# Kernel tuning notes

Hardware: AMD Instinct MI355X
Metric: run time of the kernel (lower is better)

## Reference

```python
import jax, jax.numpy as jnp
import numpy as np

EPS = 1e-6
HEAD_DIM = 64
N_Q = 16
N_KV = 2

def setup_inputs() -> dict:
    key = jax.random.key(0)
    ks = jax.random.split(key, 4)
    H = 1024
    x = jax.random.normal(ks[0], (4, 8192, H), dtype=jnp.float32)
    ln_weight = jnp.zeros((H,), dtype=jnp.float32)  # Gemma param; scale is (1 + w)
    wq = jax.random.normal(ks[1], (H, HEAD_DIM * N_Q), dtype=jnp.float32) / np.sqrt(H)
    wk = jax.random.normal(ks[2], (H, HEAD_DIM * N_KV), dtype=jnp.float32) / np.sqrt(H)
    wv = jax.random.normal(ks[3], (H, HEAD_DIM * N_KV), dtype=jnp.float32) / np.sqrt(H)
    return {"x": x, "ln_weight": ln_weight, "wq": wq, "wk": wk, "wv": wv}

def gemma_rms_norm(x, w):
    xf = x.astype(jnp.float32)
    h = xf * jax.lax.rsqrt(jnp.mean(xf * xf, axis=-1, keepdims=True) + EPS)
    return (h * (1.0 + w.astype(jnp.float32))).astype(x.dtype)

def reference(x, ln_weight, wq, wk, wv):
    # Gemma RMSNorm prologue, then three linear projections (no bias).
    h = gemma_rms_norm(x, ln_weight)            # [B, S, H]
    q = jnp.einsum('bsh,hd->bsd', h, wq)        # [B, S, nq*d]
    k = jnp.einsum('bsh,hd->bsd', h, wk)        # [B, S, nkv*d]
    v = jnp.einsum('bsh,hd->bsd', h, wv)
    B, S = x.shape[0], x.shape[1]
    q = q.reshape(B, S, N_Q, HEAD_DIM)
    k = k.reshape(B, S, N_KV, HEAD_DIM)
    v = v.reshape(B, S, N_KV, HEAD_DIM)
    return (q, k, v)
```

## Files before the change

kernel.cpp:

```cpp
#include <hip/hip_runtime.h>
#include <hip/hip_bf16.h>

typedef __attribute__((ext_vector_type(4))) float f32x4;
typedef __attribute__((ext_vector_type(8))) short bf16x8;

#define H 1024
#define NTOT 1280
#define BM 128
#define BN 256
#define BK 64
#define NKT 16
#define NTILES 5

static __device__ __forceinline__ unsigned short f2bf(float f) {
    __hip_bfloat16 b = __float2bfloat16(f);
    return __builtin_bit_cast(unsigned short, b);
}

#define GLOAD_LDS16(g, l)                                                     \
    __builtin_amdgcn_global_load_lds(                                         \
        (const __attribute__((address_space(1))) void*)(g),                   \
        (__attribute__((address_space(3))) void*)(l), 16, 0, 0)

__global__ __launch_bounds__(256) void k_rms(const float* __restrict__ x,
                                             __hip_bfloat16* __restrict__ h) {
    const int wave = threadIdx.x >> 6;
    const int lane = threadIdx.x & 63;
    const size_t row = (size_t)blockIdx.x * 4 + wave;

    const float4* xr = (const float4*)(x + row * H);
    float4 v[4];
    float ss = 0.f;
#pragma unroll
    for (int i = 0; i < 4; ++i) {
        v[i] = xr[lane + 64 * i];
        ss += v[i].x * v[i].x + v[i].y * v[i].y + v[i].z * v[i].z + v[i].w * v[i].w;
    }
#pragma unroll
    for (int o = 1; o < 64; o <<= 1) ss += __shfl_xor(ss, o);
    const float sc = rsqrtf(ss * (1.0f / H) + 1e-6f);

    ushort4* hr = (ushort4*)(h + row * H);
#pragma unroll
    for (int i = 0; i < 4; ++i) {
        ushort4 o4;
        o4.x = f2bf(v[i].x * sc);
        o4.y = f2bf(v[i].y * sc);
        o4.z = f2bf(v[i].z * sc);
        o4.w = f2bf(v[i].w * sc);
        hr[lane + 64 * i] = o4;
    }
}

__global__ __launch_bounds__(256) void k_wprep(const float* __restrict__ wq,
                                               const float* __restrict__ wk,
                                               const float* __restrict__ wv,
                                               const float* __restrict__ lnw,
                                               __hip_bfloat16* __restrict__ Bt) {
    __shared__ float l[64][65];
    const int t = threadIdx.x;
    const int kt = blockIdx.x & 15;
    const int ntl = blockIdx.x >> 4;
    const int k0 = kt * 64, n0 = ntl * 64;
    const float* src; int ldn, nb;
    if (n0 < 1024)      { src = wq; ldn = 1024; nb = n0; }
    else if (n0 < 1152) { src = wk; ldn = 128;  nb = n0 - 1024; }
    else                { src = wv; ldn = 128;  nb = n0 - 1152; }
    const int nl = t & 63, kl = t >> 6;
#pragma unroll
    for (int i = 0; i < 16; ++i) {
        const int k = kl + i * 4;
        l[k][nl] = (1.0f + lnw[k0 + k]) * src[(size_t)(k0 + k) * ldn + nb + nl];
    }
    __syncthreads();
    const int k2 = t & 63, n2 = t >> 6;
#pragma unroll
    for (int i = 0; i < 16; ++i) {
        const int n = n2 + i * 4;
        Bt[(size_t)(n0 + n) * 1024 + k0 + k2] = __float2bfloat16(l[k2][n]);
    }
}

__global__ __launch_bounds__(512, 2) void k_gemm(const __hip_bfloat16* __restrict__ A,
                                                 const __hip_bfloat16* __restrict__ Bt,
                                                 float* __restrict__ out, int rows) {
    __shared__ __align__(16) char smem[98304];

    const int tid = threadIdx.x;
    const int lane = tid & 63;
    const int wid = tid >> 6;
    const int wm = wid >> 1;
    const int wn = wid & 1;

    const int cpx = gridDim.x >> 3;
    const int wg = (blockIdx.x & 7) * cpx + (blockIdx.x >> 3);
    const int nt = wg % NTILES;
    const int mt = wg / NTILES;
    const size_t m0 = (size_t)mt * BM;

    const int cswz = ((tid & 7) * 16) ^ (((tid >> 3) & 7) << 4);
    const char* aG = (const char*)A + (m0 + (tid >> 3)) * (size_t)(H * 2) + cswz;
    const char* bG = (const char*)Bt + ((size_t)nt * BN + (tid >> 3)) * (size_t)(H * 2) + cswz;

#define STAGE_A2(buf, kt)                                                     \
    { GLOAD_LDS16(aG + (size_t)(kt) * 128,                                    \
                  smem + (buf) * 49152 + tid * 16);                           \
      GLOAD_LDS16(aG + (size_t)(kt) * 128 + (size_t)64 * (H * 2),             \
                  smem + (buf) * 49152 + 8192 + tid * 16); }
#define STAGE_B02(buf, kt)                                                    \
    { GLOAD_LDS16(bG + (size_t)(kt) * 128,                                    \
                  smem + (buf) * 49152 + 16384 + tid * 16);                   \
      GLOAD_LDS16(bG + (size_t)(kt) * 128 + (size_t)128 * (H * 2),            \
                  smem + (buf) * 49152 + 16384 + 16384 + tid * 16); }
#define STAGE_B13(buf, kt)                                                    \
    { GLOAD_LDS16(bG + (size_t)(kt) * 128 + (size_t)64 * (H * 2),             \
                  smem + (buf) * 49152 + 16384 + 8192 + tid * 16);            \
      GLOAD_LDS16(bG + (size_t)(kt) * 128 + (size_t)192 * (H * 2),            \
                  smem + (buf) * 49152 + 16384 + 24576 + tid * 16); }

    const int rowA = wm * 32 + (lane & 15);
    const int rowB = wn * 128 + (lane & 15);
    const int xm = (lane & 7) << 4;
    const int c0 = (((lane >> 4) * 16)) ^ xm;
    const int c1 = (64 + ((lane >> 4) * 16)) ^ xm;

    f32x4 acc[2][8] = {};

#define MFMAP(AK0, AK1, B0, B1, NIOFF)                                        \
    _Pragma("unroll") for (int mi = 0; mi < 2; ++mi)                          \
        _Pragma("unroll") for (int ni = 0; ni < 4; ++ni)                      \
            acc[mi][(NIOFF) + ni] = __builtin_amdgcn_mfma_f32_16x16x32_bf16(  \
                AK0[mi], B0[ni], acc[mi][(NIOFF) + ni], 0, 0, 0);             \
    _Pragma("unroll") for (int mi = 0; mi < 2; ++mi)                          \
        _Pragma("unroll") for (int ni = 0; ni < 4; ++ni)                      \
            acc[mi][(NIOFF) + ni] = __builtin_amdgcn_mfma_f32_16x16x32_bf16(  \
                AK1[mi], B1[ni], acc[mi][(NIOFF) + ni], 0, 0, 0);

#define TILE(cur, kt, CARRY, DS, VM)                                          \
    {                                                                         \
        const char* aL = smem + (cur) * 49152;                                \
        const char* bL = aL + 16384;                                          \
                                                            \
        if (CARRY) STAGE_B13((cur) ^ 1, (kt) + 1);                            \
        bf16x8 ak0[2], ak1[2], b0k0[4], b0k1[4];                              \
        _Pragma("unroll") for (int mi = 0; mi < 2; ++mi) {                    \
            ak0[mi] = *(const bf16x8*)(aL + (rowA + mi * 16) * 128 + c0);     \
            ak1[mi] = *(const bf16x8*)(aL + (rowA + mi * 16) * 128 + c1);     \
        }                                                                     \
        _Pragma("unroll") for (int ni = 0; ni < 4; ++ni) {                    \
            b0k0[ni] = *(const bf16x8*)(bL + (rowB + ni * 16) * 128 + c0);    \
            b0k1[ni] = *(const bf16x8*)(bL + (rowB + ni * 16) * 128 + c1);    \
        }                                                                     \
        asm volatile("s_waitcnt lgkmcnt(8)" ::: "memory");                    \
        __builtin_amdgcn_s_barrier();                                         \
        asm volatile("s_waitcnt lgkmcnt(0)" ::: "memory");                    \
        __builtin_amdgcn_s_setprio(1);                                        \
        MFMAP(ak0, ak1, b0k0, b0k1, 0);                                       \
        __builtin_amdgcn_s_setprio(0);                                        \
        __builtin_amdgcn_s_barrier();                                         \
                                                            \
        if (DS) { STAGE_A2(cur, (kt) + 2); STAGE_B02(cur, (kt) + 2); }        \
        bf16x8 b1k0[4], b1k1[4];                                              \
        _Pragma("unroll") for (int ni = 0; ni < 4; ++ni) {                    \
            b1k0[ni] = *(const bf16x8*)(bL + (rowB + 64 + ni * 16) * 128 + c0); \
            b1k1[ni] = *(const bf16x8*)(bL + (rowB + 64 + ni * 16) * 128 + c1); \
        }                                                                     \
        __builtin_amdgcn_s_barrier();                                         \
        asm volatile("s_waitcnt lgkmcnt(0)" ::: "memory");                    \
        __builtin_amdgcn_s_setprio(1);                                        \
        MFMAP(ak0, ak1, b1k0, b1k1, 4);                                       \
        __builtin_amdgcn_s_setprio(0);                                        \
        asm volatile("s_waitcnt vmcnt(" VM ")" ::: "memory");                 \
        __builtin_amdgcn_sched_barrier(0);                                    \
        __builtin_amdgcn_s_barrier();                                         \
        __builtin_amdgcn_sched_barrier(0);                                    \
    }

    STAGE_A2(0, 0); STAGE_B02(0, 0); STAGE_B13(0, 0);
    STAGE_A2(1, 1); STAGE_B02(1, 1); STAGE_B13(1, 1);
    asm volatile("s_waitcnt vmcnt(6)" ::: "memory");
    __builtin_amdgcn_sched_barrier(0);
    __builtin_amdgcn_s_barrier();
    __builtin_amdgcn_sched_barrier(0);

    TILE(0, 0, 0, 1, "4");
    TILE(1, 1, 1, 1, "4");
    for (int kt = 2; kt <= 12; kt += 2) {
        TILE(0, kt, 1, 1, "4");
        TILE(1, kt + 1, 1, 1, "4");
    }
    TILE(0, 14, 1, 0, "0");
    TILE(1, 15, 0, 0, "0");

    const size_t QSZ = (size_t)rows * 1024;
    const size_t KSZ = (size_t)rows * 128;
    const int colg0 = nt * BN + wn * 128;
    float* op;
    int ldc, cb0;
    if (colg0 < 1024)      { op = out;             ldc = 1024; cb0 = colg0; }
    else if (colg0 < 1152) { op = out + QSZ;       ldc = 128;  cb0 = colg0 - 1024; }
    else                   { op = out + QSZ + KSZ; ldc = 128;  cb0 = colg0 - 1152; }

    const size_t r0 = m0 + wm * 32 + ((lane >> 4) * 4);
    const int cc0 = cb0 + (lane & 15);
#pragma unroll
    for (int mi = 0; mi < 2; ++mi)
#pragma unroll
        for (int ni = 0; ni < 8; ++ni)
#pragma unroll
            for (int r = 0; r < 4; ++r)
                op[(r0 + mi * 16 + r) * (size_t)ldc + cc0 + ni * 16] = acc[mi][ni][r];
}

extern "C" void kernel_launch(void* const* d_in, const int* in_sizes, int n_in,
                              void* d_out, int out_size, void* d_ws, size_t ws_size,
                              hipStream_t stream) {
    const float* x   = (const float*)d_in[0];
    const float* lnw = (const float*)d_in[1];
    const float* wq  = (const float*)d_in[2];
    const float* wk  = (const float*)d_in[3];
    const float* wv  = (const float*)d_in[4];
    float* out = (float*)d_out;

    const int rows = in_sizes[0] / H;

    __hip_bfloat16* Bt = (__hip_bfloat16*)d_ws;
    __hip_bfloat16* h  = (__hip_bfloat16*)((char*)d_ws + (size_t)NTOT * H * 2);

    k_wprep<<<320, 256, 0, stream>>>(wq, wk, wv, lnw, Bt);
    k_rms<<<rows / 4, 256, 0, stream>>>(x, h);
    k_gemm<<<(rows / BM) * NTILES, 512, 0, stream>>>(h, Bt, out, rows);
}
```

Baseline: 151.7 us.

## Use 256x256 tiles with A staged in LDS and B loaded directly into registers

```diff
diff --git a/kernel.cpp b/kernel.cpp
--- a/kernel.cpp
+++ b/kernel.cpp
@@ -6,7 +6,7 @@
 
 #define H 1024
 #define NTOT 1280
-#define BM 128
+#define BM 256
 #define BN 256
 #define BK 64
 #define NKT 16
@@ -84,13 +84,13 @@
 __global__ __launch_bounds__(512, 2) void k_gemm(const __hip_bfloat16* __restrict__ A,
                                                  const __hip_bfloat16* __restrict__ Bt,
                                                  float* __restrict__ out, int rows) {
-    __shared__ __align__(16) char smem[98304];
+    __shared__ __align__(16) char smem[65536];
 
     const int tid = threadIdx.x;
     const int lane = tid & 63;
     const int wid = tid >> 6;
-    const int wm = wid >> 1;
-    const int wn = wid & 1;
+    const int wm = wid >> 2;
+    const int wn = wid & 3;
 
     const int cpx = gridDim.x >> 3;
     const int wg = (blockIdx.x & 7) * cpx + (blockIdx.x >> 3);
@@ -100,113 +100,92 @@
 
     const int cswz = ((tid & 7) * 16) ^ (((tid >> 3) & 7) << 4);
     const char* aG = (const char*)A + (m0 + (tid >> 3)) * (size_t)(H * 2) + cswz;
-    const char* bG = (const char*)Bt + ((size_t)nt * BN + (tid >> 3)) * (size_t)(H * 2) + cswz;
-
-#define STAGE_A2(buf, kt)                                                     \
-    { GLOAD_LDS16(aG + (size_t)(kt) * 128,                                    \
-                  smem + (buf) * 49152 + tid * 16);                           \
-      GLOAD_LDS16(aG + (size_t)(kt) * 128 + (size_t)64 * (H * 2),             \
-                  smem + (buf) * 49152 + 8192 + tid * 16); }
-#define STAGE_B02(buf, kt)                                                    \
-    { GLOAD_LDS16(bG + (size_t)(kt) * 128,                                    \
-                  smem + (buf) * 49152 + 16384 + tid * 16);                   \
-      GLOAD_LDS16(bG + (size_t)(kt) * 128 + (size_t)128 * (H * 2),            \
-                  smem + (buf) * 49152 + 16384 + 16384 + tid * 16); }
-#define STAGE_B13(buf, kt)                                                    \
-    { GLOAD_LDS16(bG + (size_t)(kt) * 128 + (size_t)64 * (H * 2),             \
-                  smem + (buf) * 49152 + 16384 + 8192 + tid * 16);            \
-      GLOAD_LDS16(bG + (size_t)(kt) * 128 + (size_t)192 * (H * 2),            \
-                  smem + (buf) * 49152 + 16384 + 24576 + tid * 16); }
-
-    const int rowA = wm * 32 + (lane & 15);
-    const int rowB = wn * 128 + (lane & 15);
+
+#define STAGE_A(buf, kt)                                                      \
+    _Pragma("unroll") for (int q = 0; q < 4; ++q)                             \
+        GLOAD_LDS16(aG + (size_t)(kt) * 128 + (size_t)q * 64 * (H * 2),       \
+                    smem + (buf) * 32768 + q * 8192 + tid * 16);
+
+    const short* bGr = (const short*)Bt
+        + ((size_t)nt * BN + wn * 64 + (lane & 15)) * (size_t)H
+        + (lane >> 4) * 8;
+
+#define BLOAD(dst, kt)                                                        \
+    _Pragma("unroll") for (int ni = 0; ni < 4; ++ni)                          \
+        _Pragma("unroll") for (int kk = 0; kk < 2; ++kk)                      \
+            dst[ni * 2 + kk] = *(const bf16x8*)(bGr + ni * 16 * H + kk * 32   \
+                                                + (size_t)(kt) * 64);
+
+    const int rowA = wm * 128 + (lane & 15);
     const int xm = (lane & 7) << 4;
     const int c0 = (((lane >> 4) * 16)) ^ xm;
     const int c1 = (64 + ((lane >> 4) * 16)) ^ xm;
 
-    f32x4 acc[2][8] = {};
-
-#define MFMAP(AK0, AK1, B0, B1, NIOFF)                                        \
-    _Pragma("unroll") for (int mi = 0; mi < 2; ++mi)                          \
-        _Pragma("unroll") for (int ni = 0; ni < 4; ++ni)                      \
-            acc[mi][(NIOFF) + ni] = __builtin_amdgcn_mfma_f32_16x16x32_bf16(  \
-                AK0[mi], B0[ni], acc[mi][(NIOFF) + ni], 0, 0, 0);             \
-    _Pragma("unroll") for (int mi = 0; mi < 2; ++mi)                          \
-        _Pragma("unroll") for (int ni = 0; ni < 4; ++ni)                      \
-            acc[mi][(NIOFF) + ni] = __builtin_amdgcn_mfma_f32_16x16x32_bf16(  \
-                AK1[mi], B1[ni], acc[mi][(NIOFF) + ni], 0, 0, 0);
-
-#define TILE(cur, kt, CARRY, DS, VM)                                          \
+    f32x4 acc[8][4] = {};
+
+#define TILE(cur, kt, BN_, DS_, bcur, bnext)                                  \
     {                                                                         \
-        const char* aL = smem + (cur) * 49152;                                \
-        const char* bL = aL + 16384;                                          \
-                                                            \
-        if (CARRY) STAGE_B13((cur) ^ 1, (kt) + 1);                            \
-        bf16x8 ak0[2], ak1[2], b0k0[4], b0k1[4];                              \
-        _Pragma("unroll") for (int mi = 0; mi < 2; ++mi) {                    \
-            ak0[mi] = *(const bf16x8*)(aL + (rowA + mi * 16) * 128 + c0);     \
-            ak1[mi] = *(const bf16x8*)(aL + (rowA + mi * 16) * 128 + c1);     \
-        }                                                                     \
-        _Pragma("unroll") for (int ni = 0; ni < 4; ++ni) {                    \
-            b0k0[ni] = *(const bf16x8*)(bL + (rowB + ni * 16) * 128 + c0);    \
-            b0k1[ni] = *(const bf16x8*)(bL + (rowB + ni * 16) * 128 + c1);    \
-        }                                                                     \
-        asm volatile("s_waitcnt lgkmcnt(8)" ::: "memory");                    \
-        __builtin_amdgcn_s_barrier();                                         \
+        if (BN_) BLOAD(bnext, (kt) + 1);                                      \
+        const char* aL = smem + (cur) * 32768;                                \
+        bf16x8 af[8];                                                         \
+        _Pragma("unroll") for (int mi = 0; mi < 8; ++mi)                      \
+            af[mi] = *(const bf16x8*)(aL + (rowA + mi * 16) * 128 + c0);      \
         asm volatile("s_waitcnt lgkmcnt(0)" ::: "memory");                    \
         __builtin_amdgcn_s_setprio(1);                                        \
-        MFMAP(ak0, ak1, b0k0, b0k1, 0);                                       \
+        _Pragma("unroll") for (int mi = 0; mi < 8; ++mi)                      \
+            _Pragma("unroll") for (int ni = 0; ni < 4; ++ni)                  \
+                acc[mi][ni] = __builtin_amdgcn_mfma_f32_16x16x32_bf16(        \
+                    af[mi], bcur[ni * 2 + 0], acc[mi][ni], 0, 0, 0);          \
         __builtin_amdgcn_s_setprio(0);                                        \
-        __builtin_amdgcn_s_barrier();                                         \
-                                                            \
-        if (DS) { STAGE_A2(cur, (kt) + 2); STAGE_B02(cur, (kt) + 2); }        \
-        bf16x8 b1k0[4], b1k1[4];                                              \
-        _Pragma("unroll") for (int ni = 0; ni < 4; ++ni) {                    \
-            b1k0[ni] = *(const bf16x8*)(bL + (rowB + 64 + ni * 16) * 128 + c0); \
-            b1k1[ni] = *(const bf16x8*)(bL + (rowB + 64 + ni * 16) * 128 + c1); \
-        }                                                                     \
-        __builtin_amdgcn_s_barrier();                                         \
+        _Pragma("unroll") for (int mi = 0; mi < 8; ++mi)                      \
+            af[mi] = *(const bf16x8*)(aL + (rowA + mi * 16) * 128 + c1);      \
         asm volatile("s_waitcnt lgkmcnt(0)" ::: "memory");                    \
         __builtin_amdgcn_s_setprio(1);                                        \
-        MFMAP(ak0, ak1, b1k0, b1k1, 4);                                       \
+        _Pragma("unroll") for (int mi = 0; mi < 8; ++mi)                      \
+            _Pragma("unroll") for (int ni = 0; ni < 4; ++ni)                  \
+                acc[mi][ni] = __builtin_amdgcn_mfma_f32_16x16x32_bf16(        \
+                    af[mi], bcur[ni * 2 + 1], acc[mi][ni], 0, 0, 0);          \
         __builtin_amdgcn_s_setprio(0);                                        \
-        asm volatile("s_waitcnt vmcnt(" VM ")" ::: "memory");                 \
+        asm volatile("s_waitcnt vmcnt(0)" ::: "memory");                      \
         __builtin_amdgcn_sched_barrier(0);                                    \
         __builtin_amdgcn_s_barrier();                                         \
         __builtin_amdgcn_sched_barrier(0);                                    \
-    }
-
-    STAGE_A2(0, 0); STAGE_B02(0, 0); STAGE_B13(0, 0);
-    STAGE_A2(1, 1); STAGE_B02(1, 1); STAGE_B13(1, 1);
-    asm volatile("s_waitcnt vmcnt(6)" ::: "memory");
+        if (DS_) STAGE_A(cur, (kt) + 2);                                      \
+    }
+
+    bf16x8 bA[8], bB[8];
+    STAGE_A(0, 0);
+    STAGE_A(1, 1);
+    BLOAD(bA, 0);
+    asm volatile("s_waitcnt vmcnt(0)" ::: "memory");
     __builtin_amdgcn_sched_barrier(0);
     __builtin_amdgcn_s_barrier();
     __builtin_amdgcn_sched_barrier(0);
 
-    TILE(0, 0, 0, 1, "4");
-    TILE(1, 1, 1, 1, "4");
-    for (int kt = 2; kt <= 12; kt += 2) {
-        TILE(0, kt, 1, 1, "4");
-        TILE(1, kt + 1, 1, 1, "4");
-    }
-    TILE(0, 14, 1, 0, "0");
-    TILE(1, 15, 0, 0, "0");
+    for (int kt = 0; kt < 12; kt += 2) {
+        TILE(0, kt, 1, 1, bA, bB);
+        TILE(1, kt + 1, 1, 1, bB, bA);
+    }
+    TILE(0, 12, 1, 1, bA, bB);
+    TILE(1, 13, 1, 1, bB, bA);
+    TILE(0, 14, 1, 0, bA, bB);
+    TILE(1, 15, 0, 0, bB, bA);
 
     const size_t QSZ = (size_t)rows * 1024;
     const size_t KSZ = (size_t)rows * 128;
-    const int colg0 = nt * BN + wn * 128;
+    const int colg0 = nt * BN + wn * 64;
     float* op;
     int ldc, cb0;
     if (colg0 < 1024)      { op = out;             ldc = 1024; cb0 = colg0; }
     else if (colg0 < 1152) { op = out + QSZ;       ldc = 128;  cb0 = colg0 - 1024; }
     else                   { op = out + QSZ + KSZ; ldc = 128;  cb0 = colg0 - 1152; }
 
-    const size_t r0 = m0 + wm * 32 + ((lane >> 4) * 4);
+    const size_t r0 = m0 + wm * 128 + ((lane >> 4) * 4);
     const int cc0 = cb0 + (lane & 15);
 #pragma unroll
-    for (int mi = 0; mi < 2; ++mi)
-#pragma unroll
-        for (int ni = 0; ni < 8; ++ni)
+    for (int mi = 0; mi < 8; ++mi)
+#pragma unroll
+        for (int ni = 0; ni < 4; ++ni)
 #pragma unroll
             for (int r = 0; r < 4; ++r)
                 op[(r0 + mi * 16 + r) * (size_t)ldc + cc0 + ni * 16] = acc[mi][ni][r];
```

Measured after the change: 199.7 us. 1.32x slower.
